# Kernel optimization log

Hardware: AMD Instinct MI355X
Metric: run time of the kernel (lower is better)

Reference implementation:

```python
import jax, jax.numpy as jnp
import numpy as np

MAX_POS = 512  # hardcoded max_pos_emb in the module
LN_EPS = 1e-5


def setup_inputs() -> dict:
    key = jax.random.key(0)
    ks = jax.random.split(key, 6)
    bs, n, d = 16, 4000, 1024
    h, dh = 8, 128
    inner = h * dh
    return {
        "x": jax.random.normal(ks[0], (bs, n, d), jnp.float32),
        "ln_w": jnp.ones((d,), jnp.float32),
        "ln_b": jnp.zeros((d,), jnp.float32),
        "Wq": (jax.random.normal(ks[1], (inner, d), jnp.float32) * 0.02),
        "Wkv": (jax.random.normal(ks[2], (2 * inner, d), jnp.float32) * 0.02),
        "Wo": (jax.random.normal(ks[3], (d, inner), jnp.float32) * 0.02),
        "bo": jnp.zeros((d,), jnp.float32),
        "rel_emb": (jax.random.normal(ks[4], (2 * MAX_POS + 1, dh), jnp.float32) * 0.02),
        "context_size": 256,
    }


def reference(x, ln_w, ln_b, Wq, Wkv, Wo, bo, rel_emb, context_size):
    bs, n, d = x.shape
    dh = rel_emb.shape[1]
    h = Wq.shape[0] // dh
    scale = dh ** -0.5
    cs = int(context_size)
    nb = -(-n // cs)          # ceil(n / cs)
    nr = n % cs

    # pre_norm (LayerNorm)
    mu = jnp.mean(x, axis=-1, keepdims=True)
    var = jnp.var(x, axis=-1, keepdims=True)
    xn = (x - mu) * jax.lax.rsqrt(var + LN_EPS) * ln_w + ln_b
    if nr > 0:
        xn = jnp.pad(xn, ((0, 0), (0, cs - nr), (0, 0)))

    q = xn @ Wq.T                    # (bs, nb*cs, h*dh)
    k, v = jnp.split(xn @ Wkv.T, 2, axis=-1)

    def blk(t):  # -> (bs, nb, h, cs, dh)
        return t.reshape(bs, nb, cs, h, dh).transpose(0, 1, 3, 2, 4)

    q, k, v = blk(q), blk(k), blk(v)

    # relative position bias, computed as a GEMM instead of broadcast-mul-sum
    seq = jnp.arange(cs)
    dist = jnp.clip(seq[:, None] - seq[None, :], -cs, cs) + MAX_POS
    rel = rel_emb[dist]                                     # (cs, cs, dh)
    pos_attn = jnp.einsum('bnhid,ijd->bnhij', q, rel) * scale

    if nr > 0:
        m = np.ones((cs, cs), dtype=bool)
        m[:nr, :nr] = False
        neg = -jnp.finfo(pos_attn.dtype).max
        pos_attn = pos_attn.at[:, -1].set(
            jnp.where(jnp.asarray(m), neg, pos_attn[:, -1]))

    # SDPA with additive mask: softmax(q k^T * scale + pos_attn) v
    scores = jnp.einsum('bnhid,bnhjd->bnhij', q, k) * scale + pos_attn
    attn = jax.nn.softmax(scores, axis=-1)
    out = jnp.einsum('bnhij,bnhjd->bnhid', attn, v)         # (bs, nb, h, cs, dh)

    out = out.transpose(0, 1, 3, 2, 4).reshape(bs, nb * cs, h * dh)[:, :n]
    return out @ Wo.T + bo  # dropout is identity in eval
```

## Files before the change

### kernel.cpp

```cpp
#include <hip/hip_runtime.h>

typedef __bf16 bf16;
typedef __bf16 bf16x8 __attribute__((ext_vector_type(8)));
typedef float f32x4 __attribute__((ext_vector_type(4)));

#define MFMA16(A,B,C) __builtin_amdgcn_mfma_f32_16x16x32_bf16(A,B,C,0,0,0)
#define SCALE 0.08838834764831843f
#define NEGBIG (-1e30f)

#define AS1(p) ((__attribute__((address_space(1))) void*)(p))
#define AS3(p) ((__attribute__((address_space(3))) void*)(p))

#define BAR() do { asm volatile("" ::: "memory"); __builtin_amdgcn_s_barrier(); asm volatile("" ::: "memory"); } while (0)

__global__ void cvt_bf16(const float* __restrict__ src, bf16* __restrict__ dst, int n) {
    int i = (blockIdx.x * 256 + threadIdx.x) * 4;
    if (i < n) {
        float4 v = *(const float4*)(src + i);
        dst[i + 0] = (bf16)v.x; dst[i + 1] = (bf16)v.y;
        dst[i + 2] = (bf16)v.z; dst[i + 3] = (bf16)v.w;
    }
}

__global__ __launch_bounds__(256) void ln_kernel(const float* __restrict__ x,
                                                 const float* __restrict__ w,
                                                 const float* __restrict__ b,
                                                 bf16* __restrict__ xn) {
    int row = blockIdx.x;
    int bb = row >> 12, p = row & 4095;
    int t = threadIdx.x;
    bf16* out = xn + ((size_t)row << 10);
    if (p >= 4000) {
        uint2 z; z.x = 0u; z.y = 0u;
        *(uint2*)(out + t * 4) = z;
        return;
    }
    float4 v = *(const float4*)(x + (((size_t)bb * 4000 + p) << 10) + t * 4);
    float s = v.x + v.y + v.z + v.w;
    float s2 = v.x * v.x + v.y * v.y + v.z * v.z + v.w * v.w;
#pragma unroll
    for (int m = 1; m < 64; m <<= 1) { s += __shfl_xor(s, m); s2 += __shfl_xor(s2, m); }
    __shared__ float red[8];
    int wv = t >> 6, l = t & 63;
    if (l == 0) { red[wv] = s; red[4 + wv] = s2; }
    __syncthreads();
    s = red[0] + red[1] + red[2] + red[3];
    s2 = red[4] + red[5] + red[6] + red[7];
    float mu = s * (1.f / 1024.f);
    float var = s2 * (1.f / 1024.f) - mu * mu;
    float inv = rsqrtf(var + 1e-5f);
    float4 wv4 = *(const float4*)(w + t * 4);
    float4 bv4 = *(const float4*)(b + t * 4);
    union { bf16 h[4]; uint2 u; } o;
    o.h[0] = (bf16)((v.x - mu) * inv * wv4.x + bv4.x);
    o.h[1] = (bf16)((v.y - mu) * inv * wv4.y + bv4.y);
    o.h[2] = (bf16)((v.z - mu) * inv * wv4.z + bv4.z);
    o.h[3] = (bf16)((v.w - mu) * inv * wv4.w + bv4.w);
    *(uint2*)(out + t * 4) = o.u;
}


__device__ __forceinline__ void stage_half(const bf16* __restrict__ src, int srow, int K,
                                           int kofs, bf16* ldsb, int w, int l) {
#pragma unroll
    for (int r = 0; r < 2; ++r) {
        int rh = (r * 8 + w) * 8 + (l >> 3);
        int chunk = (l & 7) ^ (rh & 7);
        __builtin_amdgcn_global_load_lds(AS1(src + (size_t)(srow + rh) * K + kofs + chunk * 8),
                                         AS3(ldsb + (r * 8 + w) * 512), 16, 0, 0);
    }
}

__device__ __forceinline__ bf16x8 fragLD(const bf16* base, int row, int ks, int lk) {
    int ch = ((ks * 4 + lk) ^ (row & 7)) * 8;
    return *(const bf16x8*)(base + row * 64 + ch);
}

#define RDA(AF, base, mofs) \
    _Pragma("unroll") for (int m = 0; m < 4; ++m) \
    _Pragma("unroll") for (int ks = 0; ks < 2; ++ks) \
        AF[m][ks] = fragLD(base, rA + (mofs + m) * 16 + lrow, ks, lk);

#define RDB2(nb, base) \
    _Pragma("unroll") for (int n = 0; n < 2; ++n) \
    _Pragma("unroll") for (int ks = 0; ks < 2; ++ks) \
        bfr[(nb) + n][ks] = fragLD(base, rB + ((nb) + n) * 16 + lrow, ks, lk);

#define MM(mb, AF, nb) do { \
    __builtin_amdgcn_s_setprio(1); \
    _Pragma("unroll") for (int m = 0; m < 4; ++m) \
    _Pragma("unroll") for (int n = 0; n < 2; ++n) \
    _Pragma("unroll") for (int ks = 0; ks < 2; ++ks) \
        acc[(mb) + m][(nb) + n] = MFMA16(AF[m][ks], bfr[(nb) + n][ks], acc[(mb) + m][(nb) + n]); \
    __builtin_amdgcn_s_setprio(0); } while (0)

template <int EPI>
__global__ __launch_bounds__(512, 2) void gemm256(const bf16* __restrict__ A,
                                                  const bf16* __restrict__ B,
                                                  bf16* __restrict__ C,
                                                  float* __restrict__ Cf,
                                                  const float* __restrict__ bias,
                                                  int M, int N, int K) {
    __shared__ __align__(16) bf16 LA[2 * 16384];
    __shared__ __align__(16) bf16 LB[2 * 16384];
    const int t = threadIdx.x;
    const int w = t >> 6, l = t & 63;
    const int lrow = l & 15, lk = l >> 4;
    const int wrM = w >> 2, wn = w & 3;
    const int rA = wrM * 128, rB = wn * 64;

    const int nwg = gridDim.x, cpx = nwg >> 3;
    const int swz = ((int)blockIdx.x & 7) * cpx + ((int)blockIdx.x >> 3);
    const int nbk = N >> 8;
    const int m0 = (swz / nbk) * 256;
    const int n0 = (swz % nbk) * 256;

    bf16* LA0 = LA;          bf16* LB0 = LB;
    bf16* LA1 = LA + 16384;  bf16* LB1 = LB + 16384;

    f32x4 acc[8][4] = {};
    bf16x8 afL[4][2], afH[4][2], bfr[4][2];

    const int NT = K >> 6, NI = K >> 7;

    stage_half(B, n0,       K, 0,  LB0,        w, l);
    stage_half(B, n0 + 128, K, 0,  LB0 + 8192, w, l);
    stage_half(A, m0,       K, 0,  LA0,        w, l);
    stage_half(A, m0 + 128, K, 0,  LA0 + 8192, w, l);
    stage_half(B, n0,       K, 64, LB1,        w, l);
    stage_half(B, n0 + 128, K, 64, LB1 + 8192, w, l);
    stage_half(A, m0,       K, 64, LA1,        w, l);
    asm volatile("s_waitcnt vmcnt(6)" ::: "memory");
    BAR();

    for (int i = 0; i < NI; ++i) {
        const int kS1 = (2 * i + 1) << 6;
        const int t2 = 2 * i + 2, t3 = 2 * i + 3;
        const int kS2 = ((t2 < NT) ? t2 : NT - 1) << 6;
        const int kS3 = ((t3 < NT) ? t3 : NT - 1) << 6;

        RDA(afL, LA0, 0);
        if (wn < 2) { RDB2(0, LB0); RDB2(2, LB0); } else { RDB2(0, LB0); }
        stage_half(A, m0 + 128, K, kS1, LA1 + 8192, w, l);
        BAR();
        MM(0, afL, 0);
        BAR();
        if (wn >= 2) { RDB2(2, LB0); }
        stage_half(B, n0, K, kS2, LB0, w, l);
        BAR();
        MM(0, afL, 2);
        BAR();
        RDA(afH, LA0, 4);
        stage_half(B, n0 + 128, K, kS2, LB0 + 8192, w, l);
        BAR();
        MM(4, afH, 0);
        BAR();
        stage_half(A, m0, K, kS2, LA0, w, l);
        BAR();
        MM(4, afH, 2);
        asm volatile("s_waitcnt vmcnt(6)" ::: "memory");
        BAR();
        RDA(afL, LA1, 0);
        if (wn < 2) { RDB2(0, LB1); RDB2(2, LB1); } else { RDB2(0, LB1); }
        stage_half(A, m0 + 128, K, kS2, LA0 + 8192, w, l);
        BAR();
        MM(0, afL, 0);
        BAR();
        if (wn >= 2) { RDB2(2, LB1); }
        stage_half(B, n0, K, kS3, LB1, w, l);
        BAR();
        MM(0, afL, 2);
        BAR();
        RDA(afH, LA1, 4);
        stage_half(B, n0 + 128, K, kS3, LB1 + 8192, w, l);
        BAR();
        MM(4, afH, 0);
        BAR();
        stage_half(A, m0, K, kS3, LA1, w, l);
        BAR();
        MM(4, afH, 2);
        asm volatile("s_waitcnt vmcnt(6)" ::: "memory");
        BAR();
    }

    asm volatile("s_waitcnt vmcnt(0)" ::: "memory");

    if (EPI == 0) {
#pragma unroll
        for (int m = 0; m < 8; ++m)
#pragma unroll
            for (int r = 0; r < 4; ++r) {
                size_t row = (size_t)(m0 + rA + m * 16 + lk * 4 + r);
                bf16* dst = C + row * N + n0 + rB;
#pragma unroll
                for (int n = 0; n < 4; ++n) dst[n * 16 + lrow] = (bf16)acc[m][n][r];
            }
    } else {
#pragma unroll
        for (int m = 0; m < 8; ++m)
#pragma unroll
            for (int r = 0; r < 4; ++r) {
                int row = m0 + rA + m * 16 + lk * 4 + r;
                int p = row & 4095, bb2 = row >> 12;
                if (p < 4000) {
                    float* dst = Cf + ((size_t)bb2 * 4000 + p) * 1024 + n0 + rB;
#pragma unroll
                    for (int n = 0; n < 4; ++n)
                        dst[n * 16 + lrow] = acc[m][n][r] + bias[n0 + rB + n * 16 + lrow];
                }
            }
    }
}

__global__ __launch_bounds__(512, 2) void attn_kernel(const bf16* __restrict__ qkv,
                                                      const bf16* __restrict__ relw,
                                                      bf16* __restrict__ ao) {
    int bb = blockIdx.x;
    int h = bb & 7, blkn = (bb >> 3) & 15, b = bb >> 7;
    const int t = threadIdx.x, w = t >> 6, l = t & 63, lrow = l & 15, lk = l >> 4;
    size_t qrow0 = (size_t)(b * 4096 + blkn * 256);
    __shared__ __align__(16) bf16 Ks[256 * 136];
    __shared__ __align__(16) bf16 Vt[128 * 264];
    __shared__ __align__(16) bf16 Ps[8][16 * 72];

    const int i0 = w * 32;
    const bool last = (blkn == 15);

#pragma unroll
    for (int q = 0; q < 8; ++q) {
        int idx = q * 512 + t;
        int row = idx >> 4, c8 = idx & 15;
        bf16x8 kv = *(const bf16x8*)(qkv + (qrow0 + row) * 3072 + 1024 + h * 128 + c8 * 8);
        *(bf16x8*)&Ks[row * 136 + c8 * 8] = kv;
    }
#pragma unroll
    for (int q = 0; q < 8; ++q) {
        int idx = q * 512 + t;
        int row = idx >> 4, c8 = idx & 15;
        bf16x8 vv = *(const bf16x8*)(qkv + (qrow0 + row) * 3072 + 2048 + h * 128 + c8 * 8);
        int jsw = row ^ ((c8 & 7) << 3);
#pragma unroll
        for (int e = 0; e < 8; ++e)
            Vt[(c8 * 8 + e) * 264 + jsw] = vv[e];
    }

    bf16x8 aq[2][4];
#pragma unroll
    for (int mt = 0; mt < 2; ++mt)
#pragma unroll
        for (int ks = 0; ks < 4; ++ks)
            aq[mt][ks] = *(const bf16x8*)(qkv + (qrow0 + i0 + mt * 16 + lrow) * 3072 +
                                          h * 128 + ks * 32 + lk * 8);

    f32x4 o[2][8] = {};
    float mrun[2][4], lrun[2][4];
#pragma unroll
    for (int mt = 0; mt < 2; ++mt)
#pragma unroll
        for (int r = 0; r < 4; ++r) { mrun[mt][r] = NEGBIG; lrun[mt][r] = 0.f; }

    __syncthreads();

    const int g0 = lk * 4 + 63 - lrow;
    bf16* ps = &Ps[w][0];

    for (int jt = 0; jt < 4; ++jt) {
        f32x4 s[2][4] = {};
        __builtin_amdgcn_s_setprio(1);
#pragma unroll
        for (int nt = 0; nt < 4; ++nt)
#pragma unroll
            for (int ks = 0; ks < 4; ++ks) {
                bf16x8 bk = *(const bf16x8*)&Ks[(jt * 64 + nt * 16 + lrow) * 136 +
                                                ks * 32 + lk * 8];
                s[0][nt] = MFMA16(aq[0][ks], bk, s[0][nt]);
                s[1][nt] = MFMA16(aq[1][ks], bk, s[1][nt]);
            }
        __builtin_amdgcn_s_setprio(0);

        const int cbase = i0 - jt * 64 + 192;
        f32x4 wacc[2][6] = {};
        __builtin_amdgcn_s_setprio(1);
#pragma unroll
        for (int ks = 0; ks < 4; ++ks)
#pragma unroll
            for (int ct = 0; ct < 6; ++ct) {
                bf16x8 br = *(const bf16x8*)(relw + (size_t)(cbase + ct * 16 + lrow) * 128 +
                                             ks * 32 + lk * 8);
                wacc[0][ct] = MFMA16(aq[0][ks], br, wacc[0][ct]);
                wacc[1][ct] = MFMA16(aq[1][ks], br, wacc[1][ct]);
            }
        __builtin_amdgcn_s_setprio(0);

#pragma unroll
        for (int mt = 0; mt < 2; ++mt)
#pragma unroll
            for (int r = 0; r < 4; ++r) {
                const int Kb = g0 + mt * 16 + r;
                const int dst = ((l & 48) | (Kb & 15)) << 2;
                unsigned pk[3];
#pragma unroll
                for (int P = 0; P < 3; ++P) {
                    unsigned lo = (unsigned)__builtin_bit_cast(unsigned short,
                                        (bf16)wacc[mt][2 * P][r]);
                    unsigned hi = (unsigned)__builtin_bit_cast(unsigned short,
                                        (bf16)wacc[mt][2 * P + 1][r]);
                    pk[P] = (unsigned)__builtin_amdgcn_ds_permute(dst, (int)((hi << 16) | lo));
                }
#pragma unroll
                for (int nt = 0; nt < 4; ++nt) {
                    int bcc = Kb - 16 * nt;
                    unsigned rec = (bcc < 32) ? pk[0] : (bcc < 64) ? pk[1] : pk[2];
                    unsigned b16v = ((bcc >> 4) & 1) ? (rec >> 16) : (rec & 0xffffu);
                    float wvf = __builtin_bit_cast(float, b16v << 16);
                    float xv = (s[mt][nt][r] + wvf) * SCALE;
                    if (last && (i0 + mt * 16 + lk * 4 + r >= 160 ||
                                 jt * 64 + nt * 16 + lrow >= 160))
                        xv = NEGBIG;
                    s[mt][nt][r] = xv;
                }
            }

#pragma unroll
        for (int mt = 0; mt < 2; ++mt)
#pragma unroll
            for (int r = 0; r < 4; ++r) {
                float mx = fmaxf(fmaxf(s[mt][0][r], s[mt][1][r]),
                                 fmaxf(s[mt][2][r], s[mt][3][r]));
#pragma unroll
                for (int d = 1; d < 16; d <<= 1) mx = fmaxf(mx, __shfl_xor(mx, d));
                float mold = mrun[mt][r];
                float mn = fmaxf(mold, mx);
                float corr = __expf(mold - mn);
                mrun[mt][r] = mn;
                float rs = 0.f;
#pragma unroll
                for (int nt = 0; nt < 4; ++nt) {
                    float e = __expf(s[mt][nt][r] - mn);
                    s[mt][nt][r] = e; rs += e;
                }
#pragma unroll
                for (int d = 1; d < 16; d <<= 1) rs += __shfl_xor(rs, d);
                lrun[mt][r] = lrun[mt][r] * corr + rs;
#pragma unroll
                for (int dt = 0; dt < 8; ++dt) o[mt][dt][r] *= corr;
            }

#pragma unroll
        for (int mt = 0; mt < 2; ++mt) {
#pragma unroll
            for (int nt = 0; nt < 4; ++nt)
#pragma unroll
                for (int r = 0; r < 4; ++r)
                    ps[(lk * 4 + r) * 72 + nt * 16 + lrow] = (bf16)s[mt][nt][r];
            __builtin_amdgcn_s_setprio(1);
#pragma unroll
            for (int pks = 0; pks < 2; ++pks) {
                bf16x8 ap = *(const bf16x8*)&ps[lrow * 72 + pks * 32 + lk * 8];
#pragma unroll
                for (int dt = 0; dt < 8; ++dt) {
                    int d = dt * 16 + lrow;
                    int jch = ((jt * 64 + pks * 32 + lk * 8) >> 3) ^ ((d >> 3) & 7);
                    bf16x8 bv = *(const bf16x8*)&Vt[d * 264 + (jch << 3)];
                    o[mt][dt] = MFMA16(ap, bv, o[mt][dt]);
                }
            }
            __builtin_amdgcn_s_setprio(0);
        }
    }

#pragma unroll
    for (int mt = 0; mt < 2; ++mt)
#pragma unroll
        for (int r = 0; r < 4; ++r) {
            float inv = 1.0f / lrun[mt][r];
            size_t arow = qrow0 + i0 + mt * 16 + lk * 4 + r;
            bf16* dst = ao + arow * 1024 + h * 128;
#pragma unroll
            for (int dt = 0; dt < 8; ++dt)
                dst[dt * 16 + lrow] = (bf16)(o[mt][dt][r] * inv);
        }
}

extern "C" void kernel_launch(void* const* d_in, const int* in_sizes, int n_in,
                              void* d_out, int out_size, void* d_ws, size_t ws_size,
                              hipStream_t stream) {
    const float* x   = (const float*)d_in[0];
    const float* lnw = (const float*)d_in[1];
    const float* lnb = (const float*)d_in[2];
    const float* Wq  = (const float*)d_in[3];
    const float* Wkv = (const float*)d_in[4];
    const float* Wo  = (const float*)d_in[5];
    const float* bo  = (const float*)d_in[6];
    const float* rel = (const float*)d_in[7];

    const size_t OFF_XN   = 0;
    const size_t OFF_QKV  = OFF_XN + 134217728ULL;
    const size_t OFF_WCAT = OFF_QKV + 402653184ULL;
    const size_t OFF_WO   = OFF_WCAT + 6291456ULL;
    const size_t OFF_RELW = OFF_WO + 2097152ULL;
    const size_t NEED     = OFF_RELW + 131072ULL;
    if (ws_size < NEED) return;

    char* ws = (char*)d_ws;
    bf16* xn   = (bf16*)(ws + OFF_XN);
    bf16* qkv  = (bf16*)(ws + OFF_QKV);
    bf16* wcat = (bf16*)(ws + OFF_WCAT);
    bf16* wo   = (bf16*)(ws + OFF_WO);
    bf16* relw = (bf16*)(ws + OFF_RELW);
    bf16* ao   = xn;
    float* out = (float*)d_out;

    cvt_bf16<<<1024, 256, 0, stream>>>(Wq, wcat, 1048576);
    cvt_bf16<<<2048, 256, 0, stream>>>(Wkv, wcat + 1048576, 2097152);
    cvt_bf16<<<1024, 256, 0, stream>>>(Wo, wo, 1048576);
    cvt_bf16<<<64, 256, 0, stream>>>(rel + 257 * 128, relw, 65536);
    ln_kernel<<<65536, 256, 0, stream>>>(x, lnw, lnb, xn);
    gemm256<0><<<3072, 512, 0, stream>>>(xn, wcat, qkv, nullptr, nullptr, 65536, 3072, 1024);
    attn_kernel<<<2048, 512, 0, stream>>>(qkv, relw, ao);
    gemm256<1><<<1024, 512, 0, stream>>>(ao, wo, nullptr, out, bo, 65536, 1024, 1024);
}
```

Baseline: 1.044 ms.

## Make GEMMs persistent over N tiles with continuous K-pipeline across tiles

Each GEMM workgroup now owns one 256-row M block and walks all N tiles sequentially. The staging pipeline runs across tile boundaries so that prefetch continues, and the epilogue is emitted after every 16 K-steps. The grid drops to 256 workgroups, which removes per-tile pipeline warmup and drain and keeps the A rows hot in L2. The trade-off is that 256 workgroups may underfill the machine at 2 waves per CU, and the old L2-friendly block swizzle is gone.

```diff
diff --git a/kernel.cpp b/kernel.cpp
--- a/kernel.cpp
+++ b/kernel.cpp
@@ -94,13 +94,18 @@
         acc[(mb) + m][(nb) + n] = MFMA16(AF[m][ks], bfr[(nb) + n][ks], acc[(mb) + m][(nb) + n]); \
     __builtin_amdgcn_s_setprio(0); } while (0)
 
+#define SBs(g, hf, dstb) do { int gc = (g) > GMAX ? GMAX : (g); \
+    stage_half(B, (((gc) >> 4) << 8) + (hf) * 128, K, ((gc) & 15) << 6, (dstb), w, l); } while (0)
+#define SAs(g, hf, dstb) do { int gc = (g) > GMAX ? GMAX : (g); \
+    stage_half(A, m0 + (hf) * 128, K, ((gc) & 15) << 6, (dstb), w, l); } while (0)
+
 template <int EPI>
 __global__ __launch_bounds__(512, 2) void gemm256(const bf16* __restrict__ A,
                                                   const bf16* __restrict__ B,
                                                   bf16* __restrict__ C,
                                                   float* __restrict__ Cf,
                                                   const float* __restrict__ bias,
-                                                  int M, int N, int K) {
+                                                  int ntile, int N, int K) {
     __shared__ __align__(16) bf16 LA[2 * 16384];
     __shared__ __align__(16) bf16 LB[2 * 16384];
     const int t = threadIdx.x;
@@ -108,12 +113,7 @@
     const int lrow = l & 15, lk = l >> 4;
     const int wrM = w >> 2, wn = w & 3;
     const int rA = wrM * 128, rB = wn * 64;
-
-    const int nwg = gridDim.x, cpx = nwg >> 3;
-    const int swz = ((int)blockIdx.x & 7) * cpx + ((int)blockIdx.x >> 3);
-    const int nbk = N >> 8;
-    const int m0 = (swz / nbk) * 256;
-    const int n0 = (swz % nbk) * 256;
+    const int m0 = (int)blockIdx.x << 8;
 
     bf16* LA0 = LA;          bf16* LB0 = LB;
     bf16* LA1 = LA + 16384;  bf16* LB1 = LB + 16384;
@@ -121,95 +121,84 @@
     f32x4 acc[8][4] = {};
     bf16x8 afL[4][2], afH[4][2], bfr[4][2];
 
-    const int NT = K >> 6, NI = K >> 7;
-
-    stage_half(B, n0,       K, 0,  LB0,        w, l);
-    stage_half(B, n0 + 128, K, 0,  LB0 + 8192, w, l);
-    stage_half(A, m0,       K, 0,  LA0,        w, l);
-    stage_half(A, m0 + 128, K, 0,  LA0 + 8192, w, l);
-    stage_half(B, n0,       K, 64, LB1,        w, l);
-    stage_half(B, n0 + 128, K, 64, LB1 + 8192, w, l);
-    stage_half(A, m0,       K, 64, LA1,        w, l);
+    const int GMAX = ntile * 16 - 1;
+
+    SBs(0, 0, LB0); SBs(0, 1, LB0 + 8192);
+    SAs(0, 0, LA0); SAs(0, 1, LA0 + 8192);
+    SBs(1, 0, LB1); SBs(1, 1, LB1 + 8192);
+    SAs(1, 0, LA1);
     asm volatile("s_waitcnt vmcnt(6)" ::: "memory");
     BAR();
 
-    for (int i = 0; i < NI; ++i) {
-        const int kS1 = (2 * i + 1) << 6;
-        const int t2 = 2 * i + 2, t3 = 2 * i + 3;
-        const int kS2 = ((t2 < NT) ? t2 : NT - 1) << 6;
-        const int kS3 = ((t3 < NT) ? t3 : NT - 1) << 6;
+    const int NG2 = ntile * 8;
+    for (int g2 = 0; g2 < NG2; ++g2) {
+        const int gE = 2 * g2;
 
         RDA(afL, LA0, 0);
         if (wn < 2) { RDB2(0, LB0); RDB2(2, LB0); } else { RDB2(0, LB0); }
-        stage_half(A, m0 + 128, K, kS1, LA1 + 8192, w, l);
-        BAR();
-        MM(0, afL, 0);
-        BAR();
+        SAs(gE + 1, 1, LA1 + 8192);
+        BAR(); MM(0, afL, 0); BAR();
         if (wn >= 2) { RDB2(2, LB0); }
-        stage_half(B, n0, K, kS2, LB0, w, l);
-        BAR();
-        MM(0, afL, 2);
-        BAR();
+        SBs(gE + 2, 0, LB0);
+        BAR(); MM(0, afL, 2); BAR();
         RDA(afH, LA0, 4);
-        stage_half(B, n0 + 128, K, kS2, LB0 + 8192, w, l);
-        BAR();
-        MM(4, afH, 0);
-        BAR();
-        stage_half(A, m0, K, kS2, LA0, w, l);
-        BAR();
-        MM(4, afH, 2);
+        SBs(gE + 2, 1, LB0 + 8192);
+        BAR(); MM(4, afH, 0); BAR();
+        SAs(gE + 2, 0, LA0);
+        BAR(); MM(4, afH, 2);
         asm volatile("s_waitcnt vmcnt(6)" ::: "memory");
         BAR();
         RDA(afL, LA1, 0);
         if (wn < 2) { RDB2(0, LB1); RDB2(2, LB1); } else { RDB2(0, LB1); }
-        stage_half(A, m0 + 128, K, kS2, LA0 + 8192, w, l);
-        BAR();
-        MM(0, afL, 0);
-        BAR();
+        SAs(gE + 2, 1, LA0 + 8192);
+        BAR(); MM(0, afL, 0); BAR();
         if (wn >= 2) { RDB2(2, LB1); }
-        stage_half(B, n0, K, kS3, LB1, w, l);
-        BAR();
-        MM(0, afL, 2);
-        BAR();
+        SBs(gE + 3, 0, LB1);
+        BAR(); MM(0, afL, 2); BAR();
         RDA(afH, LA1, 4);
-        stage_half(B, n0 + 128, K, kS3, LB1 + 8192, w, l);
-        BAR();
-        MM(4, afH, 0);
-        BAR();
-        stage_half(A, m0, K, kS3, LA1, w, l);
-        BAR();
-        MM(4, afH, 2);
+        SBs(gE + 3, 1, LB1 + 8192);
+        BAR(); MM(4, afH, 0); BAR();
+        SAs(gE + 3, 0, LA1);
+        BAR(); MM(4, afH, 2);
         asm volatile("s_waitcnt vmcnt(6)" ::: "memory");
         BAR();
-    }
-
+
+        if ((g2 & 7) == 7) {
+            const int n0 = (gE >> 4) << 8;
+            if (EPI == 0) {
+#pragma unroll
+                for (int m = 0; m < 8; ++m)
+#pragma unroll
+                    for (int r = 0; r < 4; ++r) {
+                        size_t row = (size_t)(m0 + rA + m * 16 + lk * 4 + r);
+                        bf16* dst = C + row * N + n0 + rB;
+#pragma unroll
+                        for (int n = 0; n < 4; ++n) dst[n * 16 + lrow] = (bf16)acc[m][n][r];
+                    }
+            } else {
+#pragma unroll
+                for (int m = 0; m < 8; ++m)
+#pragma unroll
+                    for (int r = 0; r < 4; ++r) {
+                        int row = m0 + rA + m * 16 + lk * 4 + r;
+                        int p = row & 4095, bb2 = row >> 12;
+                        if (p < 4000) {
+                            float* dst = Cf + ((size_t)bb2 * 4000 + p) * 1024 + n0 + rB;
+#pragma unroll
+                            for (int n = 0; n < 4; ++n)
+                                dst[n * 16 + lrow] = acc[m][n][r] + bias[n0 + rB + n * 16 + lrow];
+                        }
+                    }
+            }
+#pragma unroll
+            for (int m = 0; m < 8; ++m)
+#pragma unroll
+                for (int n = 0; n < 4; ++n)
+#pragma unroll
+                    for (int r2 = 0; r2 < 4; ++r2) acc[m][n][r2] = 0.f;
+        }
+    }
     asm volatile("s_waitcnt vmcnt(0)" ::: "memory");
-
-    if (EPI == 0) {
-#pragma unroll
-        for (int m = 0; m < 8; ++m)
-#pragma unroll
-            for (int r = 0; r < 4; ++r) {
-                size_t row = (size_t)(m0 + rA + m * 16 + lk * 4 + r);
-                bf16* dst = C + row * N + n0 + rB;
-#pragma unroll
-                for (int n = 0; n < 4; ++n) dst[n * 16 + lrow] = (bf16)acc[m][n][r];
-            }
-    } else {
-#pragma unroll
-        for (int m = 0; m < 8; ++m)
-#pragma unroll
-            for (int r = 0; r < 4; ++r) {
-                int row = m0 + rA + m * 16 + lk * 4 + r;
-                int p = row & 4095, bb2 = row >> 12;
-                if (p < 4000) {
-                    float* dst = Cf + ((size_t)bb2 * 4000 + p) * 1024 + n0 + rB;
-#pragma unroll
-                    for (int n = 0; n < 4; ++n)
-                        dst[n * 16 + lrow] = acc[m][n][r] + bias[n0 + rB + n * 16 + lrow];
-                }
-            }
-    }
 }
 
 __global__ __launch_bounds__(512, 2) void attn_kernel(const bf16* __restrict__ qkv,
@@ -416,7 +405,7 @@
     cvt_bf16<<<1024, 256, 0, stream>>>(Wo, wo, 1048576);
     cvt_bf16<<<64, 256, 0, stream>>>(rel + 257 * 128, relw, 65536);
     ln_kernel<<<65536, 256, 0, stream>>>(x, lnw, lnb, xn);
-    gemm256<0><<<3072, 512, 0, stream>>>(xn, wcat, qkv, nullptr, nullptr, 65536, 3072, 1024);
+    gemm256<0><<<256, 512, 0, stream>>>(xn, wcat, qkv, nullptr, nullptr, 12, 3072, 1024);
     attn_kernel<<<2048, 512, 0, stream>>>(qkv, relw, ao);
-    gemm256<1><<<1024, 512, 0, stream>>>(ao, wo, nullptr, out, bo, 65536, 1024, 1024);
-}
+    gemm256<1><<<256, 512, 0, stream>>>(ao, wo, nullptr, out, bo, 4, 1024, 1024);
+}
```

After: 1.153 ms. 1.1x slower.

## Precompute relative-position bias once per wave and fold scale into Wq

Applied to the files above, without the earlier changes.

The relative-position GEMM tiles are now computed once before the key loop, covering all 18 column tiles needed for the wave's rows, instead of recomputing 6 tiles per key tile for each of the 4 key tiles. The permuted bias values are kept in registers (72 packed words) and selected per key tile. The softmax scale is folded into Wq during bf16 conversion, which removes the per-element multiply. This cuts redundant MFMA work on the bias, at the cost of much higher register pressure, which could lower occupancy or cause spills.

```diff
diff --git a/kernel.cpp b/kernel.cpp
--- a/kernel.cpp
+++ b/kernel.cpp
@@ -13,12 +13,13 @@
 
 #define BAR() do { asm volatile("" ::: "memory"); __builtin_amdgcn_s_barrier(); asm volatile("" ::: "memory"); } while (0)
 
-__global__ void cvt_bf16(const float* __restrict__ src, bf16* __restrict__ dst, int n) {
+__global__ void cvt_bf16(const float* __restrict__ src, bf16* __restrict__ dst, int n,
+                         float scale) {
     int i = (blockIdx.x * 256 + threadIdx.x) * 4;
     if (i < n) {
         float4 v = *(const float4*)(src + i);
-        dst[i + 0] = (bf16)v.x; dst[i + 1] = (bf16)v.y;
-        dst[i + 2] = (bf16)v.z; dst[i + 3] = (bf16)v.w;
+        dst[i + 0] = (bf16)(v.x * scale); dst[i + 1] = (bf16)(v.y * scale);
+        dst[i + 2] = (bf16)(v.z * scale); dst[i + 3] = (bf16)(v.w * scale);
     }
 }
 
@@ -252,6 +253,34 @@
             aq[mt][ks] = *(const bf16x8*)(qkv + (qrow0 + i0 + mt * 16 + lrow) * 3072 +
                                           h * 128 + ks * 32 + lk * 8);
 
+    const int g0 = lk * 4 + 63 - lrow;
+
+    unsigned pkp[2][4][9];
+#pragma unroll
+    for (int mt = 0; mt < 2; ++mt) {
+        f32x4 wacc[18] = {};
+#pragma unroll
+        for (int ks = 0; ks < 4; ++ks)
+#pragma unroll
+            for (int ct = 0; ct < 18; ++ct) {
+                bf16x8 br = *(const bf16x8*)(relw + (size_t)(i0 + ct * 16 + lrow) * 128 +
+                                             ks * 32 + lk * 8);
+                wacc[ct] = MFMA16(aq[mt][ks], br, wacc[ct]);
+            }
+#pragma unroll
+        for (int r = 0; r < 4; ++r) {
+            const int dst = ((l & 48) | ((g0 + mt * 16 + r) & 15)) << 2;
+#pragma unroll
+            for (int P = 0; P < 9; ++P) {
+                unsigned lo = (unsigned)__builtin_bit_cast(unsigned short,
+                                    (bf16)wacc[2 * P][r]);
+                unsigned hi = (unsigned)__builtin_bit_cast(unsigned short,
+                                    (bf16)wacc[2 * P + 1][r]);
+                pkp[mt][r][P] = (unsigned)__builtin_amdgcn_ds_permute(dst, (int)((hi << 16) | lo));
+            }
+        }
+    }
+
     f32x4 o[2][8] = {};
     float mrun[2][4], lrun[2][4];
 #pragma unroll
@@ -261,7 +290,6 @@
 
     __syncthreads();
 
-    const int g0 = lk * 4 + 63 - lrow;
     bf16* ps = &Ps[w][0];
 
     for (int jt = 0; jt < 4; ++jt) {
@@ -278,48 +306,24 @@
             }
         __builtin_amdgcn_s_setprio(0);
 
-        const int cbase = i0 - jt * 64 + 192;
-        f32x4 wacc[2][6] = {};
-        __builtin_amdgcn_s_setprio(1);
-#pragma unroll
-        for (int ks = 0; ks < 4; ++ks)
-#pragma unroll
-            for (int ct = 0; ct < 6; ++ct) {
-                bf16x8 br = *(const bf16x8*)(relw + (size_t)(cbase + ct * 16 + lrow) * 128 +
-                                             ks * 32 + lk * 8);
-                wacc[0][ct] = MFMA16(aq[0][ks], br, wacc[0][ct]);
-                wacc[1][ct] = MFMA16(aq[1][ks], br, wacc[1][ct]);
-            }
-        __builtin_amdgcn_s_setprio(0);
-
 #pragma unroll
         for (int mt = 0; mt < 2; ++mt)
 #pragma unroll
-            for (int r = 0; r < 4; ++r) {
-                const int Kb = g0 + mt * 16 + r;
-                const int dst = ((l & 48) | (Kb & 15)) << 2;
-                unsigned pk[3];
-#pragma unroll
-                for (int P = 0; P < 3; ++P) {
-                    unsigned lo = (unsigned)__builtin_bit_cast(unsigned short,
-                                        (bf16)wacc[mt][2 * P][r]);
-                    unsigned hi = (unsigned)__builtin_bit_cast(unsigned short,
-                                        (bf16)wacc[mt][2 * P + 1][r]);
-                    pk[P] = (unsigned)__builtin_amdgcn_ds_permute(dst, (int)((hi << 16) | lo));
-                }
+            for (int r = 0; r < 4; ++r)
 #pragma unroll
                 for (int nt = 0; nt < 4; ++nt) {
-                    int bcc = Kb - 16 * nt;
-                    unsigned rec = (bcc < 32) ? pk[0] : (bcc < 64) ? pk[1] : pk[2];
-                    unsigned b16v = ((bcc >> 4) & 1) ? (rec >> 16) : (rec & 0xffffu);
-                    float wvf = __builtin_bit_cast(float, b16v << 16);
-                    float xv = (s[mt][nt][r] + wvf) * SCALE;
+                    const int base = mt * 16 + r - 16 * nt - 64 * jt + 192;
+                    const int P0 = (48 + base) >> 5, P1 = (75 + base) >> 5;
+                    int fcc = g0 + base;
+                    unsigned rec = (P0 == P1) ? pkp[mt][r][P0]
+                                 : (((fcc >> 5) == P0) ? pkp[mt][r][P0] : pkp[mt][r][P1]);
+                    unsigned b16v = ((fcc >> 4) & 1) ? (rec >> 16) : (rec & 0xffffu);
+                    float xv = s[mt][nt][r] + __builtin_bit_cast(float, b16v << 16);
                     if (last && (i0 + mt * 16 + lk * 4 + r >= 160 ||
                                  jt * 64 + nt * 16 + lrow >= 160))
                         xv = NEGBIG;
                     s[mt][nt][r] = xv;
                 }
-            }
 
 #pragma unroll
         for (int mt = 0; mt < 2; ++mt)
@@ -411,10 +415,10 @@
     bf16* ao   = xn;
     float* out = (float*)d_out;
 
-    cvt_bf16<<<1024, 256, 0, stream>>>(Wq, wcat, 1048576);
-    cvt_bf16<<<2048, 256, 0, stream>>>(Wkv, wcat + 1048576, 2097152);
-    cvt_bf16<<<1024, 256, 0, stream>>>(Wo, wo, 1048576);
-    cvt_bf16<<<64, 256, 0, stream>>>(rel + 257 * 128, relw, 65536);
+    cvt_bf16<<<1024, 256, 0, stream>>>(Wq, wcat, 1048576, SCALE);
+    cvt_bf16<<<2048, 256, 0, stream>>>(Wkv, wcat + 1048576, 2097152, 1.0f);
+    cvt_bf16<<<1024, 256, 0, stream>>>(Wo, wo, 1048576, 1.0f);
+    cvt_bf16<<<64, 256, 0, stream>>>(rel + 257 * 128, relw, 65536, 1.0f);
     ln_kernel<<<65536, 256, 0, stream>>>(x, lnw, lnb, xn);
     gemm256<0><<<3072, 512, 0, stream>>>(xn, wcat, qkv, nullptr, nullptr, 65536, 3072, 1024);
     attn_kernel<<<2048, 512, 0, stream>>>(qkv, relw, ao);
```

After: 1.177 ms. +12.7%, slower.
